# Kernel tuning notes

Hardware: AMD Instinct MI355X
Metric: run time of the kernel (lower is better)

Reference implementation:

```python
import jax, jax.numpy as jnp
import numpy as np

D_MODEL = 1024
N_LAYER = 4
D_INNER = 2048   # expand * d_model
D_STATE = 16
D_CONV = 4
DT_RANK = 64     # ceil(d_model / 16)
B, L = 2, 1024
EPS = 1e-5


def setup_inputs() -> dict:
    key = jax.random.key(0)
    ks = jax.random.split(key, 10)
    nl = N_LAYER
    def nrm(k, shape, s=0.02):
        return jax.random.normal(k, shape, jnp.float32) * s
    A_log = jnp.broadcast_to(jnp.log(jnp.arange(1, D_STATE + 1, dtype=jnp.float32)),
                             (nl, D_INNER, D_STATE)) + jnp.zeros((nl, D_INNER, D_STATE), jnp.float32)
    return {
        "hidden_states": jax.random.normal(ks[0], (B, L, D_MODEL), jnp.float32),
        "in_proj_w": nrm(ks[1], (nl, 2 * D_INNER, D_MODEL)),
        "conv_w": nrm(ks[2], (nl, D_INNER, D_CONV), 0.1),
        "conv_b": nrm(ks[3], (nl, D_INNER), 0.02),
        "x_proj_w": nrm(ks[4], (nl, DT_RANK + 2 * D_STATE, D_INNER)),
        "dt_proj_w": nrm(ks[5], (nl, D_INNER, DT_RANK), DT_RANK ** -0.5),
        "dt_proj_b": jnp.log(jnp.expm1(jax.random.uniform(ks[6], (nl, D_INNER), jnp.float32, 1e-3, 0.1))),
        "A_log": A_log,
        "D": jnp.ones((nl, D_INNER), jnp.float32),
        "out_proj_w": nrm(ks[7], (nl, D_MODEL, D_INNER)),
        "norm_w": jnp.ones((nl, D_MODEL), jnp.float32),
        "norm_b": jnp.zeros((nl, D_MODEL), jnp.float32),
        "normf_w": jnp.ones((D_MODEL,), jnp.float32),
        "normf_b": jnp.zeros((D_MODEL,), jnp.float32),
    }


def _layernorm(x, w, b):
    mu = x.mean(-1, keepdims=True)
    var = ((x - mu) ** 2).mean(-1, keepdims=True)
    return (x - mu) * jax.lax.rsqrt(var + EPS) * w + b


def _mamba(h, iw, cw, cb, xw, dw, db, Alog, Dp, ow):
    Bn, Ln, _ = h.shape
    xz = jnp.einsum('bld,ed->ble', h, iw)          # [B,L,2*d_inner]
    x, z = jnp.split(xz, 2, axis=-1)
    # depthwise causal conv1d over time, kernel size D_CONV
    xp = jnp.pad(x, ((0, 0), (D_CONV - 1, 0), (0, 0)))
    xc = sum(xp[:, k:k + Ln, :] * cw[:, k] for k in range(D_CONV)) + cb
    x = jax.nn.silu(xc)
    dbl = jnp.einsum('bld,ed->ble', x, xw)         # [B,L,dt_rank+2*d_state]
    dt = dbl[..., :DT_RANK]
    Bm = dbl[..., DT_RANK:DT_RANK + D_STATE]
    Cm = dbl[..., DT_RANK + D_STATE:]
    dt = jax.nn.softplus(jnp.einsum('blr,dr->bld', dt, dw) + db)  # [B,L,d_inner]
    A = -jnp.exp(Alog)                              # [d_inner,d_state]

    def step(hc, inp):
        dt_t, B_t, C_t, x_t = inp                   # [B,d],[B,s],[B,s],[B,d]
        dA = jnp.exp(dt_t[:, :, None] * A)
        hc = hc * dA + (dt_t * x_t)[:, :, None] * B_t[:, None, :]
        y_t = jnp.einsum('bds,bs->bd', hc, C_t)
        return hc, y_t

    h0 = jnp.zeros((Bn, D_INNER, D_STATE), x.dtype)
    xs = (dt.transpose(1, 0, 2), Bm.transpose(1, 0, 2),
          Cm.transpose(1, 0, 2), x.transpose(1, 0, 2))
    _, ys = jax.lax.scan(step, h0, xs)              # ys: [L,B,d_inner]
    y = ys.transpose(1, 0, 2) + x * Dp
    y = y * jax.nn.silu(z)
    return jnp.einsum('bld,ed->ble', y, ow)


def reference(hidden_states, in_proj_w, conv_w, conv_b, x_proj_w, dt_proj_w,
              dt_proj_b, A_log, D, out_proj_w, norm_w, norm_b, normf_w, normf_b):
    hs = hidden_states
    residual = None
    for i in range(N_LAYER):
        residual = hs if residual is None else hs + residual
        hs = _layernorm(residual, norm_w[i], norm_b[i])
        hs = _mamba(hs, in_proj_w[i], conv_w[i], conv_b[i], x_proj_w[i],
                    dt_proj_w[i], dt_proj_b[i], A_log[i], D[i], out_proj_w[i])
    residual = hs + residual
    return _layernorm(residual, normf_w, normf_b)
```

## Files before the change

kernel.cpp:

```cpp
#include <hip/hip_runtime.h>
#include <math.h>

#define D_MODEL 1024
#define D_INNER 2048
#define D_STATE 16
#define D_CONV  4
#define DT_RANK 64
#define NB      2
#define LSEQ    1024
#define NROWS   (NB * LSEQ)
#define LN_EPS  1e-5f
#define N_LAYER 4
#define NCHUNK  32
#define TCH     (LSEQ / NCHUNK)

__device__ inline unsigned bfbits(float f) {
    unsigned u = __float_as_uint(f);
    return (u + 0x7fffu + ((u >> 16) & 1u)) >> 16;
}

__device__ inline float wave_sum(float s) {
    #pragma unroll
    for (int m = 1; m < 64; m <<= 1) s += __shfl_xor(s, m, 64);
    return s;
}

__global__ __launch_bounds__(256)
void add_ln_kernel(const float* __restrict__ add, float* __restrict__ residual,
                   const float* __restrict__ w, const float* __restrict__ b,
                   void* __restrict__ out, int first, int bf16out)
{
    int row = blockIdx.x;
    int tid = threadIdx.x;
    size_t base = (size_t)row * D_MODEL + tid * 4;

    float4 v = *(const float4*)(add + base);
    if (!first) {
        float4 r = *(const float4*)(residual + base);
        v.x += r.x; v.y += r.y; v.z += r.z; v.w += r.w;
    }
    *(float4*)(residual + base) = v;

    __shared__ float red[8];
    float s = v.x + v.y + v.z + v.w;
    s = wave_sum(s);
    if ((tid & 63) == 0) red[tid >> 6] = s;
    __syncthreads();
    float mu = (red[0] + red[1] + red[2] + red[3]) * (1.0f / D_MODEL);

    float dx = v.x - mu, dy = v.y - mu, dz = v.z - mu, dw2 = v.w - mu;
    float s2 = dx*dx + dy*dy + dz*dz + dw2*dw2;
    s2 = wave_sum(s2);
    if ((tid & 63) == 0) red[4 + (tid >> 6)] = s2;
    __syncthreads();
    float var = (red[4] + red[5] + red[6] + red[7]) * (1.0f / D_MODEL);
    float rs = rsqrtf(var + LN_EPS);

    float4 wv = *(const float4*)(w + tid * 4);
    float4 bv = *(const float4*)(b + tid * 4);
    float4 o;
    o.x = dx  * rs * wv.x + bv.x;
    o.y = dy  * rs * wv.y + bv.y;
    o.z = dz  * rs * wv.z + bv.z;
    o.w = dw2 * rs * wv.w + bv.w;
    if (bf16out) {
        ushort4 ov;
        ov.x = (unsigned short)bfbits(o.x);
        ov.y = (unsigned short)bfbits(o.y);
        ov.z = (unsigned short)bfbits(o.z);
        ov.w = (unsigned short)bfbits(o.w);
        *(ushort4*)((unsigned short*)out + base) = ov;
    } else {
        *(float4*)((float*)out + base) = o;
    }
}

__global__ __launch_bounds__(256)
void f32_to_bf16_kernel(const float* __restrict__ src, unsigned short* __restrict__ dst)
{
    int i = blockIdx.x * 256 + threadIdx.x;
    float4 v = *(const float4*)(src + (size_t)i * 4);
    ushort4 o;
    o.x = (unsigned short)bfbits(v.x);
    o.y = (unsigned short)bfbits(v.y);
    o.z = (unsigned short)bfbits(v.z);
    o.w = (unsigned short)bfbits(v.w);
    *(ushort4*)(dst + (size_t)i * 4) = o;
}

__device__ inline void hl_split4(float4 v, ushort4* h4, ushort4* l4)
{
    ushort4 h, l;
    float f;
    h.x = (unsigned short)bfbits(v.x); f = __uint_as_float((unsigned)h.x << 16); l.x = (unsigned short)bfbits(v.x - f);
    h.y = (unsigned short)bfbits(v.y); f = __uint_as_float((unsigned)h.y << 16); l.y = (unsigned short)bfbits(v.y - f);
    h.z = (unsigned short)bfbits(v.z); f = __uint_as_float((unsigned)h.z << 16); l.z = (unsigned short)bfbits(v.z - f);
    h.w = (unsigned short)bfbits(v.w); f = __uint_as_float((unsigned)h.w << 16); l.w = (unsigned short)bfbits(v.w - f);
    *h4 = h; *l4 = l;
}

__global__ __launch_bounds__(256)
void prep_layer(const float* __restrict__ iw, unsigned short* __restrict__ wbuf_in,
                const float* __restrict__ xw, unsigned short* __restrict__ xwh,
                unsigned short* __restrict__ xwl,
                const float* __restrict__ dw, unsigned short* __restrict__ dwh,
                unsigned short* __restrict__ dwl,
                float* __restrict__ dbl)
{
    int b = blockIdx.x;
    int tid = threadIdx.x;
    if (b < 4096) {
        int i = b * 256 + tid;
        float4 v = *(const float4*)(iw + (size_t)i * 4);
        ushort4 o;
        o.x = (unsigned short)bfbits(v.x);
        o.y = (unsigned short)bfbits(v.y);
        o.z = (unsigned short)bfbits(v.z);
        o.w = (unsigned short)bfbits(v.w);
        *(ushort4*)(wbuf_in + (size_t)i * 4) = o;
    } else if (b < 4288) {
        int i = (b - 4096) * 256 + tid;
        float4 v = *(const float4*)(xw + (size_t)i * 4);
        hl_split4(v, (ushort4*)(xwh + (size_t)i * 4), (ushort4*)(xwl + (size_t)i * 4));
    } else if (b < 4416) {
        int i = (b - 4288) * 256 + tid;
        float4 v = *(const float4*)(dw + (size_t)i * 4);
        hl_split4(v, (ushort4*)(dwh + (size_t)i * 4), (ushort4*)(dwl + (size_t)i * 4));
    } else {
        int i = (b - 4416) * 256 + tid;
        *(float4*)(dbl + (size_t)i * 4) = make_float4(0.f, 0.f, 0.f, 0.f);
    }
}

__global__ __launch_bounds__(256)
void dtlow_hl_kernel(const float* __restrict__ dbl, unsigned short* __restrict__ hi,
                     unsigned short* __restrict__ lo)
{
    int idx = blockIdx.x * 256 + threadIdx.x;
    int m = idx >> 4, k4 = (idx & 15) * 4;
    float4 v = *(const float4*)(dbl + (size_t)m * 96 + k4);
    hl_split4(v, (ushort4*)(hi + (size_t)m * 64 + k4), (ushort4*)(lo + (size_t)m * 64 + k4));
}

using bf16x8 = __attribute__((ext_vector_type(8))) short;
using f32x4  = __attribute__((ext_vector_type(4))) float;

#define BBM 128
#define BBN 128
#define BBK 64
#define LDS_S (BBK + 8)

__global__ __launch_bounds__(256)
void gemm_bf16_nt(const unsigned short* __restrict__ A, const unsigned short* __restrict__ Bw,
                  float* __restrict__ C, int M, int N, int K)
{
    __shared__ unsigned short As[BBM * LDS_S];
    __shared__ unsigned short Bs[BBN * LDS_S];

    int tid = threadIdx.x;
    int m0 = blockIdx.y * BBM, n0 = blockIdx.x * BBN;
    int lane = tid & 63, w = tid >> 6;
    int wm = (w >> 1) * 64, wn = (w & 1) * 64;
    int lm = lane & 15, q = lane >> 4;

    int lr = tid >> 3;
    int lc = (tid & 7) * 8;

    f32x4 acc[4][4] = {};

    for (int k0 = 0; k0 < K; k0 += BBK) {
        #pragma unroll
        for (int r = 0; r < 4; ++r) {
            int row = lr + r * 32;
            uint4 av = *(const uint4*)(A + (size_t)(m0 + row) * K + k0 + lc);
            *(uint4*)&As[row * LDS_S + lc] = av;
        }
        #pragma unroll
        for (int r = 0; r < 4; ++r) {
            int row = lr + r * 32;
            uint4 pv = *(const uint4*)(Bw + (size_t)(n0 + row) * K + k0 + lc);
            *(uint4*)&Bs[row * LDS_S + lc] = pv;
        }
        __syncthreads();
        #pragma unroll
        for (int kk = 0; kk < BBK; kk += 32) {
            bf16x8 af[4], bf[4];
            #pragma unroll
            for (int i = 0; i < 4; ++i)
                af[i] = *(const bf16x8*)&As[(wm + i * 16 + lm) * LDS_S + kk + q * 8];
            #pragma unroll
            for (int j = 0; j < 4; ++j)
                bf[j] = *(const bf16x8*)&Bs[(wn + j * 16 + lm) * LDS_S + kk + q * 8];
            #pragma unroll
            for (int i = 0; i < 4; ++i)
                #pragma unroll
                for (int j = 0; j < 4; ++j)
                    acc[i][j] = __builtin_amdgcn_mfma_f32_16x16x32_bf16(
                        af[i], bf[j], acc[i][j], 0, 0, 0);
        }
        __syncthreads();
    }

    #pragma unroll
    for (int i = 0; i < 4; ++i)
        #pragma unroll
        for (int j = 0; j < 4; ++j)
            #pragma unroll
            for (int r = 0; r < 4; ++r) {
                int row = m0 + wm + i * 16 + q * 4 + r;
                int col = n0 + wn + j * 16 + lm;
                C[(size_t)row * N + col] = acc[i][j][r];
            }
}

__global__ __launch_bounds__(256)
void xproj_hl(const unsigned short* __restrict__ Ah, const unsigned short* __restrict__ Al,
              const unsigned short* __restrict__ Bh, const unsigned short* __restrict__ Bl,
              float* __restrict__ C)
{
    int tid = threadIdx.x;
    int lane = tid & 63, w = tid >> 6;
    int lm = lane & 15, q = lane >> 4;
    int m0 = blockIdx.x * 32;
    int kb = blockIdx.y * 256;

    int wm = (w & 1) * 16;
    int wn = (w >> 1) * 48;

    size_t arow = (size_t)(m0 + wm + lm) * 2048;

    f32x4 acc[3] = {};

    #pragma unroll 2
    for (int kc = 0; kc < 8; ++kc) {
        int k = kb + kc * 32 + q * 8;
        bf16x8 ah = *(const bf16x8*)&Ah[arow + k];
        bf16x8 al = *(const bf16x8*)&Al[arow + k];
        #pragma unroll
        for (int j = 0; j < 3; ++j) {
            size_t brow = (size_t)(wn + j * 16 + lm) * 2048;
            bf16x8 bh = *(const bf16x8*)&Bh[brow + k];
            bf16x8 bl = *(const bf16x8*)&Bl[brow + k];
            acc[j] = __builtin_amdgcn_mfma_f32_16x16x32_bf16(al, bh, acc[j], 0, 0, 0);
            acc[j] = __builtin_amdgcn_mfma_f32_16x16x32_bf16(ah, bl, acc[j], 0, 0, 0);
            acc[j] = __builtin_amdgcn_mfma_f32_16x16x32_bf16(ah, bh, acc[j], 0, 0, 0);
        }
    }

    #pragma unroll
    for (int j = 0; j < 3; ++j) {
        int col = wn + j * 16 + lm;
        #pragma unroll
        for (int r = 0; r < 4; ++r) {
            int row = m0 + wm + q * 4 + r;
            atomicAdd(&C[(size_t)row * 96 + col], acc[j][r]);
        }
    }
}

__global__ __launch_bounds__(256)
void dtproj_hl(const unsigned short* __restrict__ Ah, const unsigned short* __restrict__ Al,
               const unsigned short* __restrict__ Bh, const unsigned short* __restrict__ Bl,
               const float* __restrict__ bias, float* __restrict__ dtb)
{
    int tid = threadIdx.x;
    int lane = tid & 63, w = tid >> 6;
    int lm = lane & 15, q = lane >> 4;
    int n0 = blockIdx.x * 128;
    int m0 = blockIdx.y * 64;

    size_t arow = (size_t)(m0 + w * 16 + lm) * 64;

    f32x4 acc[8] = {};

    #pragma unroll
    for (int kc = 0; kc < 2; ++kc) {
        int k = kc * 32 + q * 8;
        bf16x8 ah = *(const bf16x8*)&Ah[arow + k];
        bf16x8 al = *(const bf16x8*)&Al[arow + k];
        #pragma unroll
        for (int j = 0; j < 8; ++j) {
            size_t brow = (size_t)(n0 + j * 16 + lm) * 64;
            bf16x8 bh = *(const bf16x8*)&Bh[brow + k];
            bf16x8 bl = *(const bf16x8*)&Bl[brow + k];
            acc[j] = __builtin_amdgcn_mfma_f32_16x16x32_bf16(al, bh, acc[j], 0, 0, 0);
            acc[j] = __builtin_amdgcn_mfma_f32_16x16x32_bf16(ah, bl, acc[j], 0, 0, 0);
            acc[j] = __builtin_amdgcn_mfma_f32_16x16x32_bf16(ah, bh, acc[j], 0, 0, 0);
        }
    }

    #pragma unroll
    for (int j = 0; j < 8; ++j) {
        int col = n0 + j * 16 + lm;
        float bv = bias[col];
        #pragma unroll
        for (int r = 0; r < 4; ++r) {
            int row = m0 + w * 16 + q * 4 + r;
            float v = acc[j][r] + bv;
            v = (v > 20.f) ? v : log1pf(__expf(v));
            dtb[(size_t)row * D_INNER + col] = v;
        }
    }
}

__global__ __launch_bounds__(256)
void conv_silu_kernel(const float* __restrict__ xz, const float* __restrict__ cw,
                      const float* __restrict__ cb, float* __restrict__ xc,
                      unsigned short* __restrict__ xch, unsigned short* __restrict__ xcl)
{
    int idx = blockIdx.x * 256 + threadIdx.x;
    int d  = idx & (D_INNER - 1);
    int t  = (idx >> 11) & (LSEQ - 1);
    int bb = idx >> 21;

    const float* xcol = xz + (size_t)bb * LSEQ * 2 * D_INNER + d;
    float acc = cb[d];
    #pragma unroll
    for (int k = 0; k < D_CONV; ++k) {
        int tt = t + k - (D_CONV - 1);
        if (tt >= 0) acc += xcol[(size_t)tt * 2 * D_INNER] * cw[d * D_CONV + k];
    }
    acc = acc / (1.f + __expf(-acc));
    xc[idx] = acc;
    unsigned hb = bfbits(acc);
    xch[idx] = (unsigned short)hb;
    float hf = __uint_as_float(hb << 16);
    xcl[idx] = (unsigned short)bfbits(acc - hf);
}

#define UNPK4(dst, off, v) { dst[(off)+0]=(v).x; dst[(off)+1]=(v).y; \
                             dst[(off)+2]=(v).z; dst[(off)+3]=(v).w; }

__global__ __launch_bounds__(256)
void scan_pass1(const float* __restrict__ dtb, const float* __restrict__ xc,
                const float* __restrict__ dbl, const float* __restrict__ Alog,
                float* __restrict__ aPbuf, float* __restrict__ bAbuf)
{
    int tid  = threadIdx.x;
    int half = tid & 1;
    int blk  = blockIdx.x;
    int dg   = blk & 15;
    int c    = (blk >> 4) & (NCHUNK - 1);
    int bb   = blk >> 9;
    int d    = dg * 128 + (tid >> 1);

    float A[8];
    {
        const float* pA = Alog + (size_t)d * D_STATE + half * 8;
        float4 v0 = *(const float4*)pA;
        float4 v1 = *(const float4*)(pA + 4);
        A[0] = -__expf(v0.x); A[1] = -__expf(v0.y);
        A[2] = -__expf(v0.z); A[3] = -__expf(v0.w);
        A[4] = -__expf(v1.x); A[5] = -__expf(v1.y);
        A[6] = -__expf(v1.z); A[7] = -__expf(v1.w);
    }

    size_t rowbase = (size_t)bb * LSEQ + (size_t)c * TCH;
    const float* pdt = dtb + rowbase * D_INNER + d;
    const float* pxc = xc  + rowbase * D_INNER + d;
    const float* pbc = dbl + rowbase * 96 + DT_RANK + half * 8;

    float aP[8] = {1.f,1.f,1.f,1.f,1.f,1.f,1.f,1.f};
    float bA[8] = {0.f,0.f,0.f,0.f,0.f,0.f,0.f,0.f};

    float  dtE = pdt[0], xvE = pxc[0];
    float4 BE0 = *(const float4*)pbc;
    float4 BE1 = *(const float4*)(pbc + 4);
    float  dtO = pdt[D_INNER], xvO = pxc[D_INNER];
    float4 BO0 = *(const float4*)(pbc + 96);
    float4 BO1 = *(const float4*)(pbc + 96 + 4);

    for (int t = 0; t < TCH; t += 2) {
        int t2 = (t + 2 < TCH) ? t + 2 : TCH - 1;
        int t3 = (t + 3 < TCH) ? t + 3 : TCH - 1;
        float  dtEn = pdt[(size_t)t2 * D_INNER], xvEn = pxc[(size_t)t2 * D_INNER];
        float4 BE0n = *(const float4*)(pbc + (size_t)t2 * 96);
        float4 BE1n = *(const float4*)(pbc + (size_t)t2 * 96 + 4);
        float  dtOn = pdt[(size_t)t3 * D_INNER], xvOn = pxc[(size_t)t3 * D_INNER];
        float4 BO0n = *(const float4*)(pbc + (size_t)t3 * 96);
        float4 BO1n = *(const float4*)(pbc + (size_t)t3 * 96 + 4);

        {
            float B[8];
            UNPK4(B, 0, BE0) UNPK4(B, 4, BE1)
            float dtx = dtE * xvE;
            #pragma unroll
            for (int s = 0; s < 8; ++s) {
                float a = __expf(dtE * A[s]);
                aP[s] *= a;
                bA[s] = bA[s] * a + dtx * B[s];
            }
        }
        {
            float B[8];
            UNPK4(B, 0, BO0) UNPK4(B, 4, BO1)
            float dtx = dtO * xvO;
            #pragma unroll
            for (int s = 0; s < 8; ++s) {
                float a = __expf(dtO * A[s]);
                aP[s] *= a;
                bA[s] = bA[s] * a + dtx * B[s];
            }
        }
        dtE = dtEn; xvE = xvEn; BE0 = BE0n; BE1 = BE1n;
        dtO = dtOn; xvO = xvOn; BO0 = BO0n; BO1 = BO1n;
    }

    float* pa = aPbuf + ((size_t)(bb * NCHUNK + c) * D_INNER + d) * D_STATE + half * 8;
    float* pb = bAbuf + ((size_t)(bb * NCHUNK + c) * D_INNER + d) * D_STATE + half * 8;
    *(float4*)(pa + 0) = make_float4(aP[0], aP[1], aP[2], aP[3]);
    *(float4*)(pa + 4) = make_float4(aP[4], aP[5], aP[6], aP[7]);
    *(float4*)(pb + 0) = make_float4(bA[0], bA[1], bA[2], bA[3]);
    *(float4*)(pb + 4) = make_float4(bA[4], bA[5], bA[6], bA[7]);
}

__global__ __launch_bounds__(256)
void scan_pass2(const float* __restrict__ dtb, const float* __restrict__ xc,
                const float* __restrict__ dbl, const float* __restrict__ xz,
                const float* __restrict__ Alog, const float* __restrict__ Dp,
                const float* __restrict__ aPbuf, const float* __restrict__ bAbuf,
                unsigned short* __restrict__ y)
{
    int tid  = threadIdx.x;
    int half = tid & 1;
    int blk  = blockIdx.x;
    int dg   = blk & 15;
    int c    = (blk >> 4) & (NCHUNK - 1);
    int bb   = blk >> 9;
    int d    = dg * 128 + (tid >> 1);

    float A[8];
    {
        const float* pA = Alog + (size_t)d * D_STATE + half * 8;
        float4 v0 = *(const float4*)pA;
        float4 v1 = *(const float4*)(pA + 4);
        A[0] = -__expf(v0.x); A[1] = -__expf(v0.y);
        A[2] = -__expf(v0.z); A[3] = -__expf(v0.w);
        A[4] = -__expf(v1.x); A[5] = -__expf(v1.y);
        A[6] = -__expf(v1.z); A[7] = -__expf(v1.w);
    }
    float Dd = Dp[d];

    float h[8] = {0.f,0.f,0.f,0.f,0.f,0.f,0.f,0.f};

    for (int cc = 0; cc < c; ++cc) {
        const float* pa = aPbuf + ((size_t)(bb * NCHUNK + cc) * D_INNER + d) * D_STATE + half * 8;
        const float* pb = bAbuf + ((size_t)(bb * NCHUNK + cc) * D_INNER + d) * D_STATE + half * 8;
        float4 a0 = *(const float4*)(pa + 0), a1 = *(const float4*)(pa + 4);
        float4 b0 = *(const float4*)(pb + 0), b1 = *(const float4*)(pb + 4);
        float av[8], bv[8];
        UNPK4(av, 0, a0) UNPK4(av, 4, a1)
        UNPK4(bv, 0, b0) UNPK4(bv, 4, b1)
        #pragma unroll
        for (int s = 0; s < 8; ++s) h[s] = h[s] * av[s] + bv[s];
    }

    size_t rowbase = (size_t)bb * LSEQ + (size_t)c * TCH;
    const float* pdt = dtb + rowbase * D_INNER + d;
    const float* pxc = xc  + rowbase * D_INNER + d;
    const float* pz  = xz  + rowbase * 2 * D_INNER + D_INNER + d;
    const float* pbc = dbl + rowbase * 96 + DT_RANK + half * 8;
    unsigned short* py = y + rowbase * D_INNER + d;

    float  dtE = pdt[0], xvE = pxc[0], zvE = pz[0];
    float4 BE0 = *(const float4*)pbc;
    float4 BE1 = *(const float4*)(pbc + 4);
    float4 CE0 = *(const float4*)(pbc + 16);
    float4 CE1 = *(const float4*)(pbc + 20);
    float  dtO = pdt[D_INNER], xvO = pxc[D_INNER], zvO = pz[2 * D_INNER];
    float4 BO0 = *(const float4*)(pbc + 96);
    float4 BO1 = *(const float4*)(pbc + 96 + 4);
    float4 CO0 = *(const float4*)(pbc + 96 + 16);
    float4 CO1 = *(const float4*)(pbc + 96 + 20);

    for (int t = 0; t < TCH; t += 2) {
        int t2 = (t + 2 < TCH) ? t + 2 : TCH - 1;
        int t3 = (t + 3 < TCH) ? t + 3 : TCH - 1;
        float  dtEn = pdt[(size_t)t2 * D_INNER], xvEn = pxc[(size_t)t2 * D_INNER];
        float  zvEn = pz[(size_t)t2 * 2 * D_INNER];
        float4 BE0n = *(const float4*)(pbc + (size_t)t2 * 96);
        float4 BE1n = *(const float4*)(pbc + (size_t)t2 * 96 + 4);
        float4 CE0n = *(const float4*)(pbc + (size_t)t2 * 96 + 16);
        float4 CE1n = *(const float4*)(pbc + (size_t)t2 * 96 + 20);
        float  dtOn = pdt[(size_t)t3 * D_INNER], xvOn = pxc[(size_t)t3 * D_INNER];
        float  zvOn = pz[(size_t)t3 * 2 * D_INNER];
        float4 BO0n = *(const float4*)(pbc + (size_t)t3 * 96);
        float4 BO1n = *(const float4*)(pbc + (size_t)t3 * 96 + 4);
        float4 CO0n = *(const float4*)(pbc + (size_t)t3 * 96 + 16);
        float4 CO1n = *(const float4*)(pbc + (size_t)t3 * 96 + 20);

        {
            float B[8], C[8];
            UNPK4(B, 0, BE0) UNPK4(B, 4, BE1)
            UNPK4(C, 0, CE0) UNPK4(C, 4, CE1)
            float dtx = dtE * xvE;
            float p = 0.f;
            #pragma unroll
            for (int s = 0; s < 8; ++s) {
                float a = __expf(dtE * A[s]);
                h[s] = h[s] * a + dtx * B[s];
                p += h[s] * C[s];
            }
            p += __shfl_xor(p, 1, 2);
            if (half == 0) {
                float sz = zvE / (1.f + __expf(-zvE));
                py[(size_t)t * D_INNER] = (unsigned short)bfbits((p + xvE * Dd) * sz);
            }
        }
        {
            float B[8], C[8];
            UNPK4(B, 0, BO0) UNPK4(B, 4, BO1)
            UNPK4(C, 0, CO0) UNPK4(C, 4, CO1)
            float dtx = dtO * xvO;
            float p = 0.f;
            #pragma unroll
            for (int s = 0; s < 8; ++s) {
                float a = __expf(dtO * A[s]);
                h[s] = h[s] * a + dtx * B[s];
                p += h[s] * C[s];
            }
            p += __shfl_xor(p, 1, 2);
            if (half == 0) {
                float sz = zvO / (1.f + __expf(-zvO));
                py[(size_t)(t + 1) * D_INNER] = (unsigned short)bfbits((p + xvO * Dd) * sz);
            }
        }
        dtE = dtEn; xvE = xvEn; zvE = zvEn;
        BE0 = BE0n; BE1 = BE1n; CE0 = CE0n; CE1 = CE1n;
        dtO = dtOn; xvO = xvOn; zvO = zvOn;
        BO0 = BO0n; BO1 = BO1n; CO0 = CO0n; CO1 = CO1n;
    }
}

extern "C" void kernel_launch(void* const* d_in, const int* in_sizes, int n_in,
                              void* d_out, int out_size, void* d_ws, size_t ws_size,
                              hipStream_t stream)
{
    const float* h_in  = (const float*)d_in[0];
    const float* iw    = (const float*)d_in[1];
    const float* cw    = (const float*)d_in[2];
    const float* cb    = (const float*)d_in[3];
    const float* xw    = (const float*)d_in[4];
    const float* dw    = (const float*)d_in[5];
    const float* db    = (const float*)d_in[6];
    const float* Alog  = (const float*)d_in[7];
    const float* Dp    = (const float*)d_in[8];
    const float* ow    = (const float*)d_in[9];
    const float* nw    = (const float*)d_in[10];
    const float* nb    = (const float*)d_in[11];
    const float* nfw   = (const float*)d_in[12];
    const float* nfb   = (const float*)d_in[13];

    float* ws = (float*)d_ws;
    float* residual = ws;
    float* hs       = residual + 2097152;
    float* xz       = hs + 2097152;
    float* xc       = xz + 8388608;
    float* dtb      = xc + 4194304;
    float* dbl      = dtb + 4194304;
    float* y        = dbl + 196608;

    float* aPbuf = hs;
    float* bAbuf = y + 2097152;

    unsigned short* wbuf_in  = (unsigned short*)y;
    unsigned short* hs_bf16  = (unsigned short*)(y + 2097152);
    unsigned short* y_bf16   = (unsigned short*)y;
    unsigned short* xc_hi    = (unsigned short*)y;
    unsigned short* xc_lo    = (unsigned short*)(y + 2097152);
    unsigned short* xwp_hi   = (unsigned short*)hs;
    unsigned short* xwp_lo   = (unsigned short*)(hs + 98304);
    unsigned short* dwp_hi   = (unsigned short*)(hs + 196608);
    unsigned short* dwp_lo   = (unsigned short*)(hs + 262144);
    unsigned short* dtl_hi   = (unsigned short*)(hs + 327680);
    unsigned short* dtl_lo   = (unsigned short*)(hs + 393216);
    unsigned short* wbuf_out = (unsigned short*)dtb;

    const float* cur_add = h_in;
    for (int i = 0; i < N_LAYER; ++i) {
        add_ln_kernel<<<NROWS, 256, 0, stream>>>(cur_add, residual,
                                                 nw + i * D_MODEL, nb + i * D_MODEL,
                                                 hs_bf16, i == 0, 1);
        prep_layer<<<4608, 256, 0, stream>>>(
            iw + (size_t)i * 2 * D_INNER * D_MODEL, wbuf_in,
            xw + (size_t)i * 96 * D_INNER, xwp_hi, xwp_lo,
            dw + (size_t)i * D_INNER * DT_RANK, dwp_hi, dwp_lo,
            dbl);
        gemm_bf16_nt<<<dim3(2 * D_INNER / BBN, NROWS / BBM), 256, 0, stream>>>(
            hs_bf16, wbuf_in, xz, NROWS, 2 * D_INNER, D_MODEL);
        conv_silu_kernel<<<NB * LSEQ * D_INNER / 256, 256, 0, stream>>>(
            xz, cw + (size_t)i * D_INNER * D_CONV, cb + i * D_INNER, xc, xc_hi, xc_lo);
        xproj_hl<<<dim3(NROWS / 32, 8), 256, 0, stream>>>(
            xc_hi, xc_lo, xwp_hi, xwp_lo, dbl);
        dtlow_hl_kernel<<<(NROWS * 16) / 256, 256, 0, stream>>>(dbl, dtl_hi, dtl_lo);
        dtproj_hl<<<dim3(D_INNER / 128, NROWS / 64), 256, 0, stream>>>(
            dtl_hi, dtl_lo, dwp_hi, dwp_lo, db + i * D_INNER, dtb);
        scan_pass1<<<NB * NCHUNK * (D_INNER / 128), 256, 0, stream>>>(
            dtb, xc, dbl, Alog + (size_t)i * D_INNER * D_STATE, aPbuf, bAbuf);
        scan_pass2<<<NB * NCHUNK * (D_INNER / 128), 256, 0, stream>>>(
            dtb, xc, dbl, xz, Alog + (size_t)i * D_INNER * D_STATE, Dp + i * D_INNER,
            aPbuf, bAbuf, y_bf16);
        f32_to_bf16_kernel<<<(D_MODEL * D_INNER) / 1024, 256, 0, stream>>>(
            ow + (size_t)i * D_MODEL * D_INNER, wbuf_out);
        gemm_bf16_nt<<<dim3(D_MODEL / BBN, NROWS / BBM), 256, 0, stream>>>(
            y_bf16, wbuf_out, hs, NROWS, D_MODEL, D_INNER);
        cur_add = hs;
    }
    add_ln_kernel<<<NROWS, 256, 0, stream>>>(hs, residual, nfw, nfb, d_out, 0, 0);
}
```

Measured before the change: 984.9 us.

## Use direct global-to-LDS loads with XOR swizzle in GEMM; fuse dt hi/lo split

The bf16 GEMM now loads tiles with global_load_lds straight into unpadded shared memory. An XOR swizzle on columns avoids bank conflicts, which replaces the register round-trip and the padded layout. Separately, the dtlow hi/lo split kernel is removed, and dtproj now reads fp32 dbl and splits it into bf16 hi/lo in registers, saving one launch and an intermediate buffer. The risk is that the redundant per-block conversion in dtproj and the correctness of the swizzle/LDS-load addressing (per-wave base plus lane offset) depend on exact hardware semantics.

```diff
diff --git a/kernel.cpp b/kernel.cpp
--- a/kernel.cpp
+++ b/kernel.cpp
@@ -18,6 +18,11 @@
     unsigned u = __float_as_uint(f);
     return (u + 0x7fffu + ((u >> 16) & 1u)) >> 16;
 }
+
+#define GLOAD_LDS16(gp, lp) \
+    __builtin_amdgcn_global_load_lds( \
+        (const __attribute__((address_space(1))) void*)(gp), \
+        (__attribute__((address_space(3))) void*)(lp), 16, 0, 0)
 
 __device__ inline float wave_sum(float s) {
     #pragma unroll
@@ -132,30 +137,19 @@
     }
 }
 
-__global__ __launch_bounds__(256)
-void dtlow_hl_kernel(const float* __restrict__ dbl, unsigned short* __restrict__ hi,
-                     unsigned short* __restrict__ lo)
-{
-    int idx = blockIdx.x * 256 + threadIdx.x;
-    int m = idx >> 4, k4 = (idx & 15) * 4;
-    float4 v = *(const float4*)(dbl + (size_t)m * 96 + k4);
-    hl_split4(v, (ushort4*)(hi + (size_t)m * 64 + k4), (ushort4*)(lo + (size_t)m * 64 + k4));
-}
-
 using bf16x8 = __attribute__((ext_vector_type(8))) short;
 using f32x4  = __attribute__((ext_vector_type(4))) float;
 
 #define BBM 128
 #define BBN 128
 #define BBK 64
-#define LDS_S (BBK + 8)
 
 __global__ __launch_bounds__(256)
 void gemm_bf16_nt(const unsigned short* __restrict__ A, const unsigned short* __restrict__ Bw,
                   float* __restrict__ C, int M, int N, int K)
 {
-    __shared__ unsigned short As[BBM * LDS_S];
-    __shared__ unsigned short Bs[BBN * LDS_S];
+    __shared__ unsigned short As[BBM * BBK];
+    __shared__ unsigned short Bs[BBN * BBK];
 
     int tid = threadIdx.x;
     int m0 = blockIdx.y * BBM, n0 = blockIdx.x * BBN;
@@ -163,34 +157,40 @@
     int wm = (w >> 1) * 64, wn = (w & 1) * 64;
     int lm = lane & 15, q = lane >> 4;
 
-    int lr = tid >> 3;
-    int lc = (tid & 7) * 8;
+    int lrow8 = lane >> 3;
+    int scol  = ((lane & 7) ^ lrow8) * 8;
 
     f32x4 acc[4][4] = {};
 
     for (int k0 = 0; k0 < K; k0 += BBK) {
         #pragma unroll
-        for (int r = 0; r < 4; ++r) {
-            int row = lr + r * 32;
-            uint4 av = *(const uint4*)(A + (size_t)(m0 + row) * K + k0 + lc);
-            *(uint4*)&As[row * LDS_S + lc] = av;
-        }
-        #pragma unroll
-        for (int r = 0; r < 4; ++r) {
-            int row = lr + r * 32;
-            uint4 pv = *(const uint4*)(Bw + (size_t)(n0 + row) * K + k0 + lc);
-            *(uint4*)&Bs[row * LDS_S + lc] = pv;
+        for (int j = 0; j < 4; ++j) {
+            int rbase = w * 32 + j * 8;
+            GLOAD_LDS16(A + (size_t)(m0 + rbase + lrow8) * K + k0 + scol,
+                        &As[rbase * BBK]);
+        }
+        #pragma unroll
+        for (int j = 0; j < 4; ++j) {
+            int rbase = w * 32 + j * 8;
+            GLOAD_LDS16(Bw + (size_t)(n0 + rbase + lrow8) * K + k0 + scol,
+                        &Bs[rbase * BBK]);
         }
         __syncthreads();
         #pragma unroll
         for (int kk = 0; kk < BBK; kk += 32) {
             bf16x8 af[4], bf[4];
             #pragma unroll
-            for (int i = 0; i < 4; ++i)
-                af[i] = *(const bf16x8*)&As[(wm + i * 16 + lm) * LDS_S + kk + q * 8];
-            #pragma unroll
-            for (int j = 0; j < 4; ++j)
-                bf[j] = *(const bf16x8*)&Bs[(wn + j * 16 + lm) * LDS_S + kk + q * 8];
+            for (int i = 0; i < 4; ++i) {
+                int row = wm + i * 16 + lm;
+                int col = (kk + q * 8) ^ ((row & 7) << 3);
+                af[i] = *(const bf16x8*)&As[row * BBK + col];
+            }
+            #pragma unroll
+            for (int j = 0; j < 4; ++j) {
+                int row = wn + j * 16 + lm;
+                int col = (kk + q * 8) ^ ((row & 7) << 3);
+                bf[j] = *(const bf16x8*)&Bs[row * BBK + col];
+            }
             #pragma unroll
             for (int i = 0; i < 4; ++i)
                 #pragma unroll
@@ -259,7 +259,7 @@
 }
 
 __global__ __launch_bounds__(256)
-void dtproj_hl(const unsigned short* __restrict__ Ah, const unsigned short* __restrict__ Al,
+void dtproj_hl(const float* __restrict__ dbl,
                const unsigned short* __restrict__ Bh, const unsigned short* __restrict__ Bl,
                const float* __restrict__ bias, float* __restrict__ dtb)
 {
@@ -269,15 +269,23 @@
     int n0 = blockIdx.x * 128;
     int m0 = blockIdx.y * 64;
 
-    size_t arow = (size_t)(m0 + w * 16 + lm) * 64;
+    const float* arow = dbl + (size_t)(m0 + w * 16 + lm) * 96;
 
     f32x4 acc[8] = {};
 
     #pragma unroll
     for (int kc = 0; kc < 2; ++kc) {
         int k = kc * 32 + q * 8;
-        bf16x8 ah = *(const bf16x8*)&Ah[arow + k];
-        bf16x8 al = *(const bf16x8*)&Al[arow + k];
+        float4 v0 = *(const float4*)(arow + k);
+        float4 v1 = *(const float4*)(arow + k + 4);
+        float vv[8] = {v0.x, v0.y, v0.z, v0.w, v1.x, v1.y, v1.z, v1.w};
+        bf16x8 ah, al;
+        #pragma unroll
+        for (int s = 0; s < 8; ++s) {
+            unsigned hb = bfbits(vv[s]);
+            ah[s] = (short)hb;
+            al[s] = (short)bfbits(vv[s] - __uint_as_float(hb << 16));
+        }
         #pragma unroll
         for (int j = 0; j < 8; ++j) {
             size_t brow = (size_t)(n0 + j * 16 + lm) * 64;
@@ -572,8 +580,6 @@
     unsigned short* xwp_lo   = (unsigned short*)(hs + 98304);
     unsigned short* dwp_hi   = (unsigned short*)(hs + 196608);
     unsigned short* dwp_lo   = (unsigned short*)(hs + 262144);
-    unsigned short* dtl_hi   = (unsigned short*)(hs + 327680);
-    unsigned short* dtl_lo   = (unsigned short*)(hs + 393216);
     unsigned short* wbuf_out = (unsigned short*)dtb;
 
     const float* cur_add = h_in;
@@ -592,9 +598,8 @@
             xz, cw + (size_t)i * D_INNER * D_CONV, cb + i * D_INNER, xc, xc_hi, xc_lo);
         xproj_hl<<<dim3(NROWS / 32, 8), 256, 0, stream>>>(
             xc_hi, xc_lo, xwp_hi, xwp_lo, dbl);
-        dtlow_hl_kernel<<<(NROWS * 16) / 256, 256, 0, stream>>>(dbl, dtl_hi, dtl_lo);
         dtproj_hl<<<dim3(D_INNER / 128, NROWS / 64), 256, 0, stream>>>(
-            dtl_hi, dtl_lo, dwp_hi, dwp_lo, db + i * D_INNER, dtb);
+            dbl, dwp_hi, dwp_lo, db + i * D_INNER, dtb);
         scan_pass1<<<NB * NCHUNK * (D_INNER / 128), 256, 0, stream>>>(
             dtb, xc, dbl, Alog + (size_t)i * D_INNER * D_STATE, aPbuf, bAbuf);
         scan_pass2<<<NB * NCHUNK * (D_INNER / 128), 256, 0, stream>>>(
```

After: 972.3 us. About the same (-1.3%).
